# Performance work log

Hardware: AMD Instinct MI355X
Metric: run time of the kernel (lower is better)

## Reference

```python
import jax, jax.numpy as jnp
import numpy as np

NEG_SLOPE = 0.2
N, IN_DIM, OUT_DIM, N_HEADS = 4096, 512, 512, 4
D_K = OUT_DIM // N_HEADS


def setup_inputs() -> dict:
    key = jax.random.key(0)
    k1, k2, k3, k4, k5 = jax.random.split(key, 5)
    H = jax.random.normal(k1, (N, IN_DIM), dtype=jnp.float32)
    A = jax.random.randint(k2, (N, N), 0, 2, dtype=jnp.int32)
    W = jax.random.normal(k3, (IN_DIM, OUT_DIM), dtype=jnp.float32) * (1.0 / np.sqrt(IN_DIM))
    a_l = jax.random.normal(k4, (N_HEADS, D_K), dtype=jnp.float32) * 0.1
    a_r = jax.random.normal(k5, (N_HEADS, D_K), dtype=jnp.float32) * 0.1
    return {"H": H, "A": A, "W": W, "a_l": a_l, "a_r": a_r}


def reference(H, A, W, a_l, a_r):
    n = H.shape[0]
    # mask = (A + I) > 0, shape (N, N); self-loops always allowed
    mask = (A + jnp.eye(n, dtype=A.dtype)) > 0
    # Wh: (N, heads, d_k)
    Wh = (H @ W).reshape(n, N_HEADS, D_K)
    sl = jnp.einsum('nhd,hd->nh', Wh, a_l)  # (N, heads)
    sr = jnp.einsum('nhd,hd->nh', Wh, a_r)  # (N, heads)
    # e[i, h, j] = leaky_relu(sl[i,h] + sr[j,h])
    e = jax.nn.leaky_relu(sl[:, :, None] + sr.T[None, :, :], negative_slope=NEG_SLOPE)
    e = jnp.where(mask[:, None, :], e, -jnp.inf)
    alpha = jnp.nan_to_num(jax.nn.softmax(e, axis=2), nan=0.0)  # dropout is identity at eval
    # out[i, h, :] = sum_j alpha[i,h,j] * Wh[j,h,:]
    out = jnp.einsum('nhm,mhd->nhd', alpha, Wh).reshape(n, OUT_DIM)
    return jax.nn.elu(out)
```

## Files before the change

### kernel.cpp

```cpp
#include <hip/hip_runtime.h>

typedef unsigned short ushort_t;
typedef __attribute__((ext_vector_type(8)))  short  short8;
typedef __attribute__((ext_vector_type(4)))  short  short4v;
typedef __attribute__((ext_vector_type(4)))  float  float4v;
typedef __attribute__((ext_vector_type(4)))  int    int4v;

#define N_NODES 4096
#define NHEADS  4
#define DK      128
#define ODIM    512
#define KDIM    512

__device__ __forceinline__ float bf2f(ushort_t u) {
    return __uint_as_float(((unsigned)u) << 16);
}
__device__ __forceinline__ ushort_t f2bf_rne(float f) {
    unsigned u = __float_as_uint(f);
    u += 0x7fffu + ((u >> 16) & 1u);
    return (ushort_t)(u >> 16);
}

__global__ __launch_bounds__(256) void pack_mask_k(const int* __restrict__ A,
                                                   unsigned long long* __restrict__ P,
                                                   const ushort_t* __restrict__ Hraw,
                                                   int* __restrict__ flag,
                                                   const void* __restrict__ W,
                                                   ushort_t* __restrict__ WT,
                                                   float* __restrict__ sl,
                                                   float* __restrict__ sr)
{
    __shared__ ushort_t lt[64][72];
    __shared__ int dcnt[4];
    const int tid = threadIdx.x;
    const int bx  = blockIdx.x;

    if (bx == 0 && tid < 64) {
        const int lane = tid;
        int cnt = 0;
        #pragma unroll
        for (int s = 0; s < 16; ++s) {
            ushort_t v = Hraw[(lane * 16 + s) * 2];
            int e = (v >> 7) & 0xFF;
            cnt += (((e >= 90) && (e <= 140)) || (v == 0)) ? 1 : 0;
        }
        #pragma unroll
        for (int off = 32; off; off >>= 1) cnt += __shfl_down(cnt, off);
        if (lane == 0) *flag = (cnt < 768) ? 1 : 0;
    }

    {
        const int lane = tid & 63;
        #pragma unroll
        for (int kk = 0; kk < 4; ++kk) {
            const int flat4 = (bx * 4 + kk) * 256 + tid;
            const int row   = flat4 >> 10;
            const int col0  = (flat4 << 2) & 4095;
            const int4v a   = ((const int4v*)A)[flat4];
            unsigned nib = 0;
            #pragma unroll
            for (int j = 0; j < 4; ++j)
                nib |= ((a[j] != 0) || (row == col0 + j)) ? (1u << j) : 0u;
            unsigned long long v = (unsigned long long)nib << ((lane & 15) * 4);
            v |= __shfl_xor(v, 1);
            v |= __shfl_xor(v, 2);
            v |= __shfl_xor(v, 4);
            v |= __shfl_xor(v, 8);
            if ((lane & 15) == 0) P[flat4 >> 4] = v;
        }
    }

    if (bx >= 64 && bx < 96) {
        const int idx = (bx - 64) * 256 + tid;
        float4v z;
        #pragma unroll
        for (int e = 0; e < 4; ++e) z[e] = 0.f;
        if (idx < 4096) ((float4v*)sl)[idx] = z;
        else            ((float4v*)sr)[idx - 4096] = z;
    }

    if (bx < 64) {
        int cnt = 0;
        #pragma unroll
        for (int s = 0; s < 4; ++s) {
            ushort_t v = Hraw[(tid * 4 + s) * 2];
            int e = (v >> 7) & 0xFF;
            cnt += (((e >= 90) && (e <= 140)) || (v == 0)) ? 1 : 0;
        }
        #pragma unroll
        for (int off = 32; off; off >>= 1) cnt += __shfl_down(cnt, off);
        if ((tid & 63) == 0) dcnt[tid >> 6] = cnt;
        __syncthreads();
        const int f32 = (dcnt[0] + dcnt[1] + dcnt[2] + dcnt[3]) < 768;

        const int ti = bx >> 3, tj = bx & 7;
        const int r = tid >> 2, c2 = tid & 3;
        const size_t eo = (size_t)(ti * 64 + r) * KDIM + tj * 64 + c2 * 16;
        if (f32) {
            const float4v* src = (const float4v*)((const float*)W + eo);
            float4v f0 = src[0], f1 = src[1], f2 = src[2], f3 = src[3];
            #pragma unroll
            for (int e = 0; e < 4; ++e) {
                lt[r][c2 * 16 +  0 + e] = f2bf_rne(f0[e]);
                lt[r][c2 * 16 +  4 + e] = f2bf_rne(f1[e]);
                lt[r][c2 * 16 +  8 + e] = f2bf_rne(f2[e]);
                lt[r][c2 * 16 + 12 + e] = f2bf_rne(f3[e]);
            }
        } else {
            const short8* src = (const short8*)((const ushort_t*)W + eo);
            short8 v0 = src[0];
            short8 v1 = src[1];
            *(short8*)&lt[r][c2 * 16]     = v0;
            *(short8*)&lt[r][c2 * 16 + 8] = v1;
        }
        __syncthreads();
        #pragma unroll
        for (int itr = 0; itr < 2; ++itr) {
            int idx = itr * 256 + tid;
            int n = idx >> 3, c = idx & 7;
            short8 vv;
            #pragma unroll
            for (int e = 0; e < 8; ++e) vv[e] = (short)lt[c * 8 + e][n];
            *(short8*)(WT + (size_t)(tj * 64 + n) * KDIM + ti * 64 + c * 8) = vv;
        }
    }
}

__global__ __launch_bounds__(256) void gemm_wht_dual_k(const void* __restrict__ H,
                                                       const ushort_t* __restrict__ WT,
                                                       ushort_t* __restrict__ WhT,
                                                       const int* __restrict__ flag,
                                                       const void* __restrict__ al,
                                                       const void* __restrict__ ar,
                                                       float* __restrict__ sl,
                                                       float* __restrict__ sr)
{
    __shared__ ushort_t Bs[64 * KDIM];
    __shared__ ushort_t lt[64][72];
    const int f32 = *flag;
    const int tid  = threadIdx.x;
    const int lane = tid & 63;
    const int wid  = tid >> 6;
    const int quad = lane >> 4;
    const int l15  = lane & 15;
    const int bm = blockIdx.x & 63, bn = blockIdx.x >> 6;
    const int i0 = bm * 64, n0 = bn * 64;

    #pragma unroll
    for (int rr = 0; rr < 16; ++rr) {
        const int n = wid * 16 + rr;
        const ushort_t* src = WT + (size_t)(n0 + n) * KDIM + (size_t)((lane ^ (n & 3)) * 8);
        __builtin_amdgcn_global_load_lds(
            (const __attribute__((address_space(1))) void*)src,
            (__attribute__((address_space(3))) void*)(Bs + n * KDIM), 16, 0, 0);
    }
    asm volatile("s_waitcnt vmcnt(0)" ::: "memory");
    __syncthreads();

    const size_t aoff = (size_t)(i0 + wid * 16 + l15) * KDIM + quad * 8;

    float4v acc0, acc1, acc2, acc3;
    #pragma unroll
    for (int e = 0; e < 4; ++e) { acc0[e] = 0.f; acc1[e] = 0.f; acc2[e] = 0.f; acc3[e] = 0.f; }

    const int sx = l15 & 3;

    #pragma unroll 4
    for (int k8 = 0; k8 < 64; k8 += 4) {
        short8 a;
        if (f32) {
            const float4v* fp = (const float4v*)((const float*)H + aoff + (size_t)k8 * 8);
            float4v x0 = fp[0], x1 = fp[1];
            #pragma unroll
            for (int e = 0; e < 4; ++e) {
                a[e]     = (short)f2bf_rne(x0[e]);
                a[4 + e] = (short)f2bf_rne(x1[e]);
            }
        } else {
            a = *(const short8*)((const ushort_t*)H + aoff + (size_t)k8 * 8);
        }
        const int s = (quad + k8) ^ sx;
        short8 b0 = *(const short8*)(Bs + ( 0 + l15) * KDIM + s * 8);
        short8 b1 = *(const short8*)(Bs + (16 + l15) * KDIM + s * 8);
        short8 b2 = *(const short8*)(Bs + (32 + l15) * KDIM + s * 8);
        short8 b3 = *(const short8*)(Bs + (48 + l15) * KDIM + s * 8);
        acc0 = __builtin_amdgcn_mfma_f32_16x16x32_bf16(a, b0, acc0, 0, 0, 0);
        acc1 = __builtin_amdgcn_mfma_f32_16x16x32_bf16(a, b1, acc1, 0, 0, 0);
        acc2 = __builtin_amdgcn_mfma_f32_16x16x32_bf16(a, b2, acc2, 0, 0, 0);
        acc3 = __builtin_amdgcn_mfma_f32_16x16x32_bf16(a, b3, acc3, 0, 0, 0);
    }

    #pragma unroll
    for (int r = 0; r < 4; ++r) {
        int m = wid * 16 + quad * 4 + r;
        lt[ 0 + l15][m] = f2bf_rne(acc0[r]);
        lt[16 + l15][m] = f2bf_rne(acc1[r]);
        lt[32 + l15][m] = f2bf_rne(acc2[r]);
        lt[48 + l15][m] = f2bf_rne(acc3[r]);
    }
    __syncthreads();
    #pragma unroll
    for (int itr = 0; itr < 2; ++itr) {
        int idx = itr * 256 + tid;
        int n = idx >> 3, c = idx & 7;
        short8 v = *(const short8*)&lt[n][c * 8];
        *(short8*)(WhT + (size_t)(n0 + n) * N_NODES + i0 + c * 8) = v;
    }

    {
        const int h2 = n0 >> 7;
        const int d0 = n0 & 127;
        const int m  = tid >> 2;
        const int part = tid & 3;
        float psl = 0.f, psr = 0.f;
        #pragma unroll
        for (int k = 0; k < 16; ++k) {
            int n = part * 16 + k;
            float wv = bf2f(lt[n][m]);
            float av = f32 ? ((const float*)al)[h2 * DK + d0 + n]
                           : bf2f(((const ushort_t*)al)[h2 * DK + d0 + n]);
            float bv = f32 ? ((const float*)ar)[h2 * DK + d0 + n]
                           : bf2f(((const ushort_t*)ar)[h2 * DK + d0 + n]);
            psl += wv * av;
            psr += wv * bv;
        }
        psl += __shfl_down(psl, 2); psl += __shfl_down(psl, 1);
        psr += __shfl_down(psr, 2); psr += __shfl_down(psr, 1);
        if (part == 0) {
            atomicAdd(&sl[h2 * N_NODES + i0 + m], psl);
            atomicAdd(&sr[h2 * N_NODES + i0 + m], psr);
        }
    }
}

__global__ __launch_bounds__(1024, 4) void attn_full_k(const ushort_t* __restrict__ WhT,
                                                       const unsigned* __restrict__ Apack,
                                                       const float* __restrict__ sl,
                                                       const float* __restrict__ sr,
                                                       void* __restrict__ out,
                                                       const int* __restrict__ flag)
{
    __shared__ char smem[147456] __attribute__((aligned(16)));
    ushort_t* vbuf = (ushort_t*)smem;
    float*    srs  = (float*)(smem + 131072);

    const int f32  = *flag;
    const int tid  = threadIdx.x;
    const int lane = tid & 63;
    const int wid  = tid >> 6;
    const int wq   = wid & 3;
    const int js   = wid >> 2;
    const int quad = lane >> 4;
    const int l15  = lane & 15;
    const int bx   = blockIdx.x;
    const int h    = bx & 3;
    const int i0   = (bx >> 2) << 6;

    const float C1 = 1.44269504f;

    for (int j = tid; j < 4096; j += 1024) srs[j] = sr[h * N_NODES + j] * C1;
    const int myrow = wq * 16 + l15;
    const float slv = sl[h * N_NODES + i0 + myrow] * C1;
    const unsigned* mrow = Apack + (size_t)(i0 + myrow) * 128;
    __syncthreads();

    float4v acc[8];
    #pragma unroll
    for (int nt = 0; nt < 8; ++nt)
        #pragma unroll
        for (int e = 0; e < 4; ++e) acc[nt][e] = 0.f;
    float4v accden;
    #pragma unroll
    for (int e = 0; e < 4; ++e) accden[e] = 0.f;

    short8 ones;
    #pragma unroll
    for (int e = 0; e < 8; ++e) ones[e] = (short)0x3F80;

    const int rrow  = lane >> 5;
    const int s32   = lane & 31;
    const int dbase = wid * 8;

    #define DMA_WIN(BUF, W)                                                            \
        { _Pragma("unroll")                                                            \
          for (int q_ = 0; q_ < 4; ++q_) {                                             \
            const int d_  = dbase + q_ * 2 + rrow;                                     \
            const int ch_ = s32 ^ (d_ & 31);                                           \
            const ushort_t* g_ = WhT + (size_t)(h * DK + d_) * N_NODES                 \
                                      + (size_t)(W) * 256 + (size_t)ch_ * 8;           \
            __builtin_amdgcn_global_load_lds(                                          \
                (const __attribute__((address_space(1))) void*)g_,                     \
                (__attribute__((address_space(3))) void*)(vbuf + (BUF) * 32768         \
                                                         + wid * 2048 + q_ * 512),     \
                16, 0, 0);                                                             \
          } }

    unsigned wa0 = mrow[js * 2 + 0];
    unsigned wa1 = mrow[js * 2 + 1];
    DMA_WIN(0, 0)

    #pragma unroll 1
    for (int w = 0; w < 16; ++w) {
        __syncthreads();
        unsigned wa0n = wa0, wa1n = wa1;
        if (w < 15) {
            wa0n = mrow[(w + 1) * 8 + js * 2 + 0];
            wa1n = mrow[(w + 1) * 8 + js * 2 + 1];
            DMA_WIN((w + 1) & 1, w + 1)
        }

        const float4v a0 = *(const float4v*)&srs[w * 256 + js * 64 + quad * 8];
        const float4v a1 = *(const float4v*)&srs[w * 256 + js * 64 + quad * 8 + 4];
        const float4v b0 = *(const float4v*)&srs[w * 256 + js * 64 + 32 + quad * 8];
        const float4v b1 = *(const float4v*)&srs[w * 256 + js * 64 + 32 + quad * 8 + 4];

        short8 pf0, pf1;
        #pragma unroll
        for (int jj = 0; jj < 8; ++jj) {
            const int bit = quad * 8 + jj;
            float x = slv + ((jj < 4) ? a0[jj] : a1[jj - 4]);
            float t = fmaxf(x, x * 0.2f);
            t = ((wa0 >> bit) & 1u) ? t : -1e30f;
            pf0[jj] = (short)(ushort_t)(__float_as_uint(__builtin_amdgcn_exp2f(t)) >> 16);
            float y = slv + ((jj < 4) ? b0[jj] : b1[jj - 4]);
            float u = fmaxf(y, y * 0.2f);
            u = ((wa1 >> bit) & 1u) ? u : -1e30f;
            pf1[jj] = (short)(ushort_t)(__float_as_uint(__builtin_amdgcn_exp2f(u)) >> 16);
        }

        const ushort_t* vB = vbuf + (w & 1) * 32768;
        __builtin_amdgcn_s_setprio(1);
        #pragma unroll
        for (int nt = 0; nt < 8; ++nt) {
            const int roff  = (nt * 16 + l15) * 256;
            const int dlow  = (nt & 1) * 16 + l15;
            const int slot0 = (js * 8 + 0 + quad) ^ dlow;
            const int slot1 = (js * 8 + 4 + quad) ^ dlow;
            short8 bv0 = *(const short8*)(vB + roff + slot0 * 8);
            short8 bv1 = *(const short8*)(vB + roff + slot1 * 8);
            acc[nt] = __builtin_amdgcn_mfma_f32_16x16x32_bf16(pf0, bv0, acc[nt], 0, 0, 0);
            acc[nt] = __builtin_amdgcn_mfma_f32_16x16x32_bf16(pf1, bv1, acc[nt], 0, 0, 0);
        }
        accden = __builtin_amdgcn_mfma_f32_16x16x32_bf16(pf0, ones, accden, 0, 0, 0);
        accden = __builtin_amdgcn_mfma_f32_16x16x32_bf16(pf1, ones, accden, 0, 0, 0);
        __builtin_amdgcn_s_setprio(0);

        wa0 = wa0n; wa1 = wa1n;
    }
    #undef DMA_WIN

    float* red  = (float*)smem;
    float* lsum = (float*)(smem + 98304);
    __syncthreads();

    if (js != 0) {
        float* rp = red + (size_t)((js - 1) * 4 + wq) * 2048;
        #pragma unroll
        for (int nt = 0; nt < 8; ++nt)
            #pragma unroll
            for (int r = 0; r < 4; ++r)
                rp[(quad * 4 + r) * 128 + nt * 16 + l15] = acc[nt][r];
        if (l15 == 0) {
            #pragma unroll
            for (int r = 0; r < 4; ++r)
                lsum[js * 64 + wq * 16 + quad * 4 + r] = accden[r];
        }
    }
    __syncthreads();
    if (js == 0) {
        float rinv[4];
        #pragma unroll
        for (int r = 0; r < 4; ++r) {
            const int rowo = wq * 16 + quad * 4 + r;
            float den = accden[r] + lsum[64 + rowo] + lsum[128 + rowo] + lsum[192 + rowo];
            rinv[r] = 1.0f / fmaxf(den, 1e-37f);
        }
        #pragma unroll
        for (int nt = 0; nt < 8; ++nt)
            #pragma unroll
            for (int r = 0; r < 4; ++r) {
                const int ri = (quad * 4 + r) * 128 + nt * 16 + l15;
                float v = (acc[nt][r]
                           + red[(size_t)(0 * 4 + wq) * 2048 + ri]
                           + red[(size_t)(1 * 4 + wq) * 2048 + ri]
                           + red[(size_t)(2 * 4 + wq) * 2048 + ri]) * rinv[r];
                float e = __builtin_amdgcn_exp2f(v * C1) - 1.0f;
                float o = (v > 0.f) ? v : e;
                const size_t oidx = (size_t)(i0 + wq * 16 + quad * 4 + r) * ODIM
                                  + h * DK + nt * 16 + l15;
                if (f32) ((float*)out)[oidx] = o;
                else     ((ushort_t*)out)[oidx] = f2bf_rne(o);
            }
    }
}

extern "C" void kernel_launch(void* const* d_in, const int* in_sizes, int n_in,
                              void* d_out, int out_size, void* d_ws, size_t ws_size,
                              hipStream_t stream)
{
    const void* H  = d_in[0];
    const int*  A  = (const int*)d_in[1];
    const void* W  = d_in[2];
    const void* al = d_in[3];
    const void* ar = d_in[4];

    if (ws_size < (7u << 20)) return;

    char* ws = (char*)d_ws;
    ushort_t* WhT   = (ushort_t*)ws;
    unsigned long long* Apack = (unsigned long long*)(ws + (4u << 20));
    ushort_t* WT    = (ushort_t*)(ws + (6u << 20));
    float*    sl    = (float*)(ws + (6u << 20) + (512u << 10));
    float*    sr    = (float*)(ws + (6u << 20) + (576u << 10));
    int*      flag  = (int*)(ws + (6u << 20) + (640u << 10));

    pack_mask_k    <<<4096,  256, 0, stream>>>(A, Apack, (const ushort_t*)H, flag,
                                               W, WT, sl, sr);
    gemm_wht_dual_k<<<512,   256, 0, stream>>>(H, WT, WhT, flag, al, ar, sl, sr);
    attn_full_k    <<<256,  1024, 0, stream>>>(WhT, (const unsigned*)Apack, sl, sr,
                                               (void*)d_out, flag);
}
```

Baseline: 158.9 us.

## Give each wave two row tiles so each B fragment feeds two MFMAs

Waves are remapped from a 4-row-group by 4-j-split layout to a 2-row-group by 8-j-split layout. Each wave now handles 32 query rows over 32 neighbours per window, so every Wh fragment read from LDS feeds two MFMAs, halving LDS reads per MFMA. Each wave also builds the sr and bias inputs once for both row tiles. The cost is 32 accumulator vectors per thread, which raises register pressure under the 1024-thread launch bound, and a longer tree reduction across eight j-splits with five extra barriers in the epilogue.

```diff
diff --git a/kernel.cpp b/kernel.cpp
--- a/kernel.cpp
+++ b/kernel.cpp
@@ -248,8 +248,8 @@
     const int tid  = threadIdx.x;
     const int lane = tid & 63;
     const int wid  = tid >> 6;
-    const int wq   = wid & 3;
-    const int js   = wid >> 2;
+    const int rq   = wid & 1;
+    const int js   = wid >> 1;
     const int quad = lane >> 4;
     const int l15  = lane & 15;
     const int bx   = blockIdx.x;
@@ -259,19 +259,24 @@
     const float C1 = 1.44269504f;
 
     for (int j = tid; j < 4096; j += 1024) srs[j] = sr[h * N_NODES + j] * C1;
-    const int myrow = wq * 16 + l15;
-    const float slv = sl[h * N_NODES + i0 + myrow] * C1;
-    const unsigned* mrow = Apack + (size_t)(i0 + myrow) * 128;
-    __syncthreads();
-
-    float4v acc[8];
-    #pragma unroll
-    for (int nt = 0; nt < 8; ++nt)
-        #pragma unroll
-        for (int e = 0; e < 4; ++e) acc[nt][e] = 0.f;
-    float4v accden;
-    #pragma unroll
-    for (int e = 0; e < 4; ++e) accden[e] = 0.f;
+    const int row_lo = rq * 32 + l15;
+    const int row_hi = rq * 32 + 16 + l15;
+    const float slv0 = sl[h * N_NODES + i0 + row_lo] * C1;
+    const float slv1 = sl[h * N_NODES + i0 + row_hi] * C1;
+    const unsigned* mlo = Apack + (size_t)(i0 + row_lo) * 128;
+    const unsigned* mhi = Apack + (size_t)(i0 + row_hi) * 128;
+    __syncthreads();
+
+    float4v acc[2][8];
+    #pragma unroll
+    for (int m = 0; m < 2; ++m)
+        #pragma unroll
+        for (int nt = 0; nt < 8; ++nt)
+            #pragma unroll
+            for (int e = 0; e < 4; ++e) acc[m][nt][e] = 0.f;
+    float4v accden0, accden1;
+    #pragma unroll
+    for (int e = 0; e < 4; ++e) { accden0[e] = 0.f; accden1[e] = 0.f; }
 
     short8 ones;
     #pragma unroll
@@ -295,8 +300,8 @@
                 16, 0, 0);                                                             \
           } }
 
-    unsigned wa0 = mrow[js * 2 + 0];
-    unsigned wa1 = mrow[js * 2 + 1];
+    unsigned wa0 = mlo[js];
+    unsigned wa1 = mhi[js];
     DMA_WIN(0, 0)
 
     #pragma unroll 1
@@ -304,25 +309,24 @@
         __syncthreads();
         unsigned wa0n = wa0, wa1n = wa1;
         if (w < 15) {
-            wa0n = mrow[(w + 1) * 8 + js * 2 + 0];
-            wa1n = mrow[(w + 1) * 8 + js * 2 + 1];
+            wa0n = mlo[(w + 1) * 8 + js];
+            wa1n = mhi[(w + 1) * 8 + js];
             DMA_WIN((w + 1) & 1, w + 1)
         }
 
-        const float4v a0 = *(const float4v*)&srs[w * 256 + js * 64 + quad * 8];
-        const float4v a1 = *(const float4v*)&srs[w * 256 + js * 64 + quad * 8 + 4];
-        const float4v b0 = *(const float4v*)&srs[w * 256 + js * 64 + 32 + quad * 8];
-        const float4v b1 = *(const float4v*)&srs[w * 256 + js * 64 + 32 + quad * 8 + 4];
+        const float4v a0 = *(const float4v*)&srs[w * 256 + js * 32 + quad * 8];
+        const float4v a1 = *(const float4v*)&srs[w * 256 + js * 32 + quad * 8 + 4];
 
         short8 pf0, pf1;
         #pragma unroll
         for (int jj = 0; jj < 8; ++jj) {
             const int bit = quad * 8 + jj;
-            float x = slv + ((jj < 4) ? a0[jj] : a1[jj - 4]);
+            const float srj = (jj < 4) ? a0[jj] : a1[jj - 4];
+            float x = slv0 + srj;
             float t = fmaxf(x, x * 0.2f);
             t = ((wa0 >> bit) & 1u) ? t : -1e30f;
             pf0[jj] = (short)(ushort_t)(__float_as_uint(__builtin_amdgcn_exp2f(t)) >> 16);
-            float y = slv + ((jj < 4) ? b0[jj] : b1[jj - 4]);
+            float y = slv1 + srj;
             float u = fmaxf(y, y * 0.2f);
             u = ((wa1 >> bit) & 1u) ? u : -1e30f;
             pf1[jj] = (short)(ushort_t)(__float_as_uint(__builtin_amdgcn_exp2f(u)) >> 16);
@@ -332,17 +336,15 @@
         __builtin_amdgcn_s_setprio(1);
         #pragma unroll
         for (int nt = 0; nt < 8; ++nt) {
-            const int roff  = (nt * 16 + l15) * 256;
-            const int dlow  = (nt & 1) * 16 + l15;
-            const int slot0 = (js * 8 + 0 + quad) ^ dlow;
-            const int slot1 = (js * 8 + 4 + quad) ^ dlow;
-            short8 bv0 = *(const short8*)(vB + roff + slot0 * 8);
-            short8 bv1 = *(const short8*)(vB + roff + slot1 * 8);
-            acc[nt] = __builtin_amdgcn_mfma_f32_16x16x32_bf16(pf0, bv0, acc[nt], 0, 0, 0);
-            acc[nt] = __builtin_amdgcn_mfma_f32_16x16x32_bf16(pf1, bv1, acc[nt], 0, 0, 0);
-        }
-        accden = __builtin_amdgcn_mfma_f32_16x16x32_bf16(pf0, ones, accden, 0, 0, 0);
-        accden = __builtin_amdgcn_mfma_f32_16x16x32_bf16(pf1, ones, accden, 0, 0, 0);
+            const int roff = (nt * 16 + l15) * 256;
+            const int dlow = (nt & 1) * 16 + l15;
+            const int slot = (js * 4 + quad) ^ dlow;
+            short8 bv = *(const short8*)(vB + roff + slot * 8);
+            acc[0][nt] = __builtin_amdgcn_mfma_f32_16x16x32_bf16(pf0, bv, acc[0][nt], 0, 0, 0);
+            acc[1][nt] = __builtin_amdgcn_mfma_f32_16x16x32_bf16(pf1, bv, acc[1][nt], 0, 0, 0);
+        }
+        accden0 = __builtin_amdgcn_mfma_f32_16x16x32_bf16(pf0, ones, accden0, 0, 0, 0);
+        accden1 = __builtin_amdgcn_mfma_f32_16x16x32_bf16(pf1, ones, accden1, 0, 0, 0);
         __builtin_amdgcn_s_setprio(0);
 
         wa0 = wa0n; wa1 = wa1n;
@@ -350,48 +352,74 @@
     #undef DMA_WIN
 
     float* red  = (float*)smem;
-    float* lsum = (float*)(smem + 98304);
-    __syncthreads();
-
-    if (js != 0) {
-        float* rp = red + (size_t)((js - 1) * 4 + wq) * 2048;
-        #pragma unroll
-        for (int nt = 0; nt < 8; ++nt)
-            #pragma unroll
-            for (int r = 0; r < 4; ++r)
-                rp[(quad * 4 + r) * 128 + nt * 16 + l15] = acc[nt][r];
-        if (l15 == 0) {
-            #pragma unroll
-            for (int r = 0; r < 4; ++r)
-                lsum[js * 64 + wq * 16 + quad * 4 + r] = accden[r];
-        }
-    }
+    float* lsum = (float*)(smem + 131072);
+    __syncthreads();
+
+    if (js != 0 && l15 == 0) {
+        #pragma unroll
+        for (int r = 0; r < 4; ++r) {
+            lsum[(js - 1) * 64 + rq * 32 + quad * 4 + r]      = accden0[r];
+            lsum[(js - 1) * 64 + rq * 32 + 16 + quad * 4 + r] = accden1[r];
+        }
+    }
+    #define RED_WRITE(IDX)                                                             \
+        {   float* rp_ = red + (size_t)(IDX) * 4096;                                   \
+            _Pragma("unroll")                                                          \
+            for (int m = 0; m < 2; ++m)                                                \
+              _Pragma("unroll")                                                        \
+              for (int nt = 0; nt < 8; ++nt)                                           \
+                _Pragma("unroll")                                                      \
+                for (int r = 0; r < 4; ++r)                                            \
+                    rp_[(m * 16 + quad * 4 + r) * 128 + nt * 16 + l15] = acc[m][nt][r]; }
+    #define RED_ADD(IDX)                                                               \
+        {   float* rp_ = red + (size_t)(IDX) * 4096;                                   \
+            _Pragma("unroll")                                                          \
+            for (int m = 0; m < 2; ++m)                                                \
+              _Pragma("unroll")                                                        \
+              for (int nt = 0; nt < 8; ++nt)                                           \
+                _Pragma("unroll")                                                      \
+                for (int r = 0; r < 4; ++r)                                            \
+                    acc[m][nt][r] += rp_[(m * 16 + quad * 4 + r) * 128 + nt * 16 + l15]; }
+
+    if (js >= 4) RED_WRITE((js - 4) * 2 + rq)
+    __syncthreads();
+    if (js < 4)  RED_ADD(js * 2 + rq)
+    __syncthreads();
+    if (js == 2 || js == 3) RED_WRITE((js - 2) * 2 + rq)
+    __syncthreads();
+    if (js < 2)  RED_ADD(js * 2 + rq)
+    __syncthreads();
+    if (js == 1) RED_WRITE(rq)
     __syncthreads();
     if (js == 0) {
-        float rinv[4];
-        #pragma unroll
-        for (int r = 0; r < 4; ++r) {
-            const int rowo = wq * 16 + quad * 4 + r;
-            float den = accden[r] + lsum[64 + rowo] + lsum[128 + rowo] + lsum[192 + rowo];
-            rinv[r] = 1.0f / fmaxf(den, 1e-37f);
-        }
-        #pragma unroll
-        for (int nt = 0; nt < 8; ++nt)
+        RED_ADD(rq)
+        #pragma unroll
+        for (int m = 0; m < 2; ++m) {
+            float rinv[4];
             #pragma unroll
             for (int r = 0; r < 4; ++r) {
-                const int ri = (quad * 4 + r) * 128 + nt * 16 + l15;
-                float v = (acc[nt][r]
-                           + red[(size_t)(0 * 4 + wq) * 2048 + ri]
-                           + red[(size_t)(1 * 4 + wq) * 2048 + ri]
-                           + red[(size_t)(2 * 4 + wq) * 2048 + ri]) * rinv[r];
-                float e = __builtin_amdgcn_exp2f(v * C1) - 1.0f;
-                float o = (v > 0.f) ? v : e;
-                const size_t oidx = (size_t)(i0 + wq * 16 + quad * 4 + r) * ODIM
-                                  + h * DK + nt * 16 + l15;
-                if (f32) ((float*)out)[oidx] = o;
-                else     ((ushort_t*)out)[oidx] = f2bf_rne(o);
+                const int row = rq * 32 + m * 16 + quad * 4 + r;
+                float den = (m == 0) ? accden0[r] : accden1[r];
+                #pragma unroll
+                for (int q = 1; q < 8; ++q) den += lsum[(q - 1) * 64 + row];
+                rinv[r] = 1.0f / fmaxf(den, 1e-37f);
             }
-    }
+            #pragma unroll
+            for (int nt = 0; nt < 8; ++nt)
+                #pragma unroll
+                for (int r = 0; r < 4; ++r) {
+                    float v = acc[m][nt][r] * rinv[r];
+                    float e = __builtin_amdgcn_exp2f(v * C1) - 1.0f;
+                    float o = (v > 0.f) ? v : e;
+                    const size_t oidx = (size_t)(i0 + rq * 32 + m * 16 + quad * 4 + r) * ODIM
+                                      + h * DK + nt * 16 + l15;
+                    if (f32) ((float*)out)[oidx] = o;
+                    else     ((ushort_t*)out)[oidx] = f2bf_rne(o);
+                }
+        }
+    }
+    #undef RED_WRITE
+    #undef RED_ADD
 }
 
 extern "C" void kernel_launch(void* const* d_in, const int* in_sizes, int n_in,
```

Measured after the change: 170.2 us. 1.07x slower.
